# Optimization experiments

Hardware: AMD Instinct MI355X
Metric: run time of the kernel (lower is better)

Reference implementation:

```python
import jax, jax.numpy as jnp
import numpy as np

B, T, P, N, U, L, K = 32, 12, 12, 512, 64, 2, 2
C = 2 * U  # combined_dim = input_dim(rnn_units) + rnn_units = 128


def setup_inputs():
    ks = jax.random.split(jax.random.key(0), 24)
    inp = {
        'x': jax.random.normal(ks[0], (B, T, N, 1), jnp.float32),
        'adj': jax.random.uniform(ks[1], (N, N), jnp.float32),
        'spatial_mask_1': 0.1 * jax.random.normal(ks[2], (N, N), jnp.float32),
        'spatial_mask_2': 0.1 * jax.random.normal(ks[3], (N, N), jnp.float32),
        'temporal_mask': 0.1 * jax.random.normal(ks[4], (T, N), jnp.float32),
        'fc_in_w': 0.1 * jax.random.normal(ks[5], (1, U), jnp.float32),
        'fc_in_b': jnp.zeros((U,), jnp.float32),
        'fc_out_w': 0.1 * jax.random.normal(ks[6], (U, 1), jnp.float32),
        'fc_out_b': jnp.zeros((1,), jnp.float32),
    }
    i = 7
    for pre in ('enc', 'dec'):
        for name, od in (('w_ru', 2 * U), ('w_c', U), ('w_ru2', 2 * U), ('w_c2', U)):
            inp[pre + '_' + name] = 0.08 * jax.random.normal(ks[i], (L, 2 * K, C, od), jnp.float32)
            i += 1
            inp[pre + '_' + name.replace('w', 'b')] = jnp.zeros((L, od), jnp.float32)
    return inp


def _supports(adj):
    # adj_hat = A + I; fwd = D_out^-1 A_hat ; bwd = D_in^-1 A_hat^T (inf -> 0)
    ah = adj + jnp.eye(adj.shape[0], dtype=adj.dtype)
    d_out = ah.sum(1)
    d_in = ah.sum(0)
    inv_out = jnp.where(d_out > 0, 1.0 / d_out, 0.0)
    inv_in = jnp.where(d_in > 0, 1.0 / d_in, 0.0)
    return inv_out[:, None] * ah, inv_in[:, None] * ah.T


def _dgc(x, sup, w, b):
    # x: [B,N,C]; sup: (fwd,bwd) each [N,N]; w: [2K,C,O]; b: [O]
    # The torch code expands x K times per support, so each k-slice of x_out is
    # identical: sum_k P_s @ w[k] == P_s @ w[sK:(s+1)K].sum(0). Same math, fused.
    pf = jnp.einsum('nm,bni->bmi', sup[0], x)
    pb = jnp.einsum('nm,bni->bmi', sup[1], x)
    return (jnp.einsum('bni,io->bno', pf, w[:K].sum(0))
            + jnp.einsum('bni,io->bno', pb, w[K:].sum(0)) + b)


def _cell(x, h, s1, s2, w_ru, b_ru, w_c, b_c, w_ru2, b_ru2, w_c2, b_c2):
    xh = jnp.concatenate([x, h], axis=-1)
    r1, u1 = jnp.split(jax.nn.sigmoid(_dgc(xh, s1, w_ru, b_ru)), 2, axis=-1)
    c1 = jnp.tanh(_dgc(jnp.concatenate([x, r1 * h], axis=-1), s1, w_c, b_c))
    r2, u2 = jnp.split(jax.nn.sigmoid(_dgc(xh, s2, w_ru2, b_ru2)), 2, axis=-1)
    c2 = jnp.tanh(_dgc(jnp.concatenate([x, r2 * h], axis=-1), s2, w_c2, b_c2))
    u = 0.5 * (u1 + u2)
    c = 0.5 * (c1 + c2)
    return (1.0 - u) * h + u * c


def _forward(x, adj, sm1, sm2, tm, fc_in_w, fc_in_b, fc_out_w, fc_out_b, enc, dec):
    x = x * (jnp.tanh(tm) + 1.0)[None, :, :, None]
    adj1 = adj * (jnp.tanh(0.5 * (sm1 + sm1.T)) + 1.0)
    adj2 = adj * (jnp.tanh(0.5 * (sm2 + sm2.T)) + 1.0)
    s1 = _supports(adj1)
    s2 = _supports(adj2)

    def run_layers(cells, inp, h):
        hs = []
        for i in range(L):
            hi = _cell(inp, h[i], s1, s2, *[p[i] for p in cells])
            hs.append(hi)
            inp = hi
        return jnp.stack(hs)

    def enc_step(h, xt):
        inp = xt @ fc_in_w + fc_in_b  # [B,N,U]
        return run_layers(enc, inp, h), None

    h0 = jnp.zeros((L, B, N, U), x.dtype)
    h, _ = jax.lax.scan(enc_step, h0, jnp.swapaxes(x, 0, 1))

    def dec_step(carry, _):
        h, go = carry
        inp = go @ fc_in_w + fc_in_b
        h = run_layers(dec, inp, h)
        out_t = h[-1] @ fc_out_w + fc_out_b  # [B,N,1]
        return (h, out_t), out_t

    _, outs = jax.lax.scan(dec_step, (h, jnp.zeros((B, N, 1), x.dtype)), None, length=P)
    return jnp.swapaxes(outs, 0, 1)[..., 0]  # [B,P,N]


def reference(x, adj, spatial_mask_1, spatial_mask_2, temporal_mask,
              fc_in_w, fc_in_b, fc_out_w, fc_out_b,
              enc_w_ru, enc_b_ru, enc_w_c, enc_b_c, enc_w_ru2, enc_b_ru2, enc_w_c2, enc_b_c2,
              dec_w_ru, dec_b_ru, dec_w_c, dec_b_c, dec_w_ru2, dec_b_ru2, dec_w_c2, dec_b_c2):
    enc = (enc_w_ru, enc_b_ru, enc_w_c, enc_b_c, enc_w_ru2, enc_b_ru2, enc_w_c2, enc_b_c2)
    dec = (dec_w_ru, dec_b_ru, dec_w_c, dec_b_c, dec_w_ru2, dec_b_ru2, dec_w_c2, dec_b_c2)
    return _forward(x, adj, spatial_mask_1, spatial_mask_2, temporal_mask,
                    fc_in_w, fc_in_b, fc_out_w, fc_out_b, enc, dec)
```

## Files before the change

kernel.cpp:

```cpp
#include <hip/hip_runtime.h>
#include <math.h>

#define NN 512
#define BB 32
#define UU 64
#define CC 128
#define TT 12
#define NP 12
#define RRR (NN*BB)

typedef _Float16 f16;
typedef f16 f16x8 __attribute__((ext_vector_type(8)));
typedef f16 f16x4 __attribute__((ext_vector_type(4)));
typedef float f32x4 __attribute__((ext_vector_type(4)));

__device__ __forceinline__ void gload16(const f16* g, f16* l) {
  __builtin_amdgcn_global_load_lds((const __attribute__((address_space(1))) void*)g,
                                   (__attribute__((address_space(3))) void*)l, 16, 0, 0);
}

static const size_t OFF_ST    = 0;
static const size_t OFF_AH    = OFF_ST   + (size_t)4*512*512;
static const size_t OFF_INVD  = OFF_AH   + (size_t)2*512*512;
static const size_t OFF_XH    = OFF_INVD + 2048;
static const size_t OFF_H     = OFF_XH   + (size_t)2*RRR*CC;
static const size_t OFF_RH    = OFF_H    + (size_t)2*RRR*UU;
static const size_t OFF_U     = OFF_RH   + (size_t)2*RRR*UU;
static const size_t OFF_CB    = OFF_U    + (size_t)2*RRR*UU;
static const size_t OFF_F16   = OFF_CB   + (size_t)2*RRR*UU;
static const size_t OFF_ST16A = OFF_F16;
static const size_t OFF_ST16B = OFF_ST16A + 524288;
static const size_t OFF_XHT1  = OFF_ST16B + 524288;
static const size_t OFF_XHT2  = OFF_XHT1  + 1048576;
static const size_t OFF_RHT1  = OFF_XHT2  + 1048576;
static const size_t OFF_RHT2  = OFF_RHT1  + 1048576;
static const size_t OFF_P1    = OFF_RHT2  + 1048576;
static const size_t OFF_P2    = OFF_P1    + 4194304;
static const size_t OFF_Q1    = OFF_P2    + 4194304;
static const size_t OFF_Q2    = OFF_Q1    + 2097152;
static const size_t OFF_WT1   = OFF_Q2    + 2097152;
static const size_t OFF_WT2   = OFF_WT1   + 196608;

__global__ void k_build_ah(const float* __restrict__ adj, const float* __restrict__ sm1,
                           const float* __restrict__ sm2, float* __restrict__ ah) {
  int a = blockIdx.y, i = blockIdx.x;
  const float* sm = a ? sm2 : sm1;
  for (int j = threadIdx.x; j < NN; j += blockDim.x) {
    float m = tanhf(0.5f * (sm[i*NN + j] + sm[j*NN + i])) + 1.0f;
    ah[((size_t)a*NN + i)*NN + j] = adj[i*NN + j] * m + ((i == j) ? 1.0f : 0.0f);
  }
}

__global__ void k_deg(const float* __restrict__ ah, float* __restrict__ invd) {
  int a = blockIdx.y, n = blockIdx.x;
  const float* A = ah + (size_t)a*NN*NN;
  __shared__ float sr[256], sc[256];
  int t = threadIdx.x;
  sr[t] = A[(size_t)n*NN + t] + A[(size_t)n*NN + t + 256];
  sc[t] = A[(size_t)t*NN + n] + A[(size_t)(t+256)*NN + n];
  __syncthreads();
  for (int s = 128; s > 0; s >>= 1) {
    if (t < s) { sr[t] += sr[t+s]; sc[t] += sc[t+s]; }
    __syncthreads();
  }
  if (t == 0) {
    float dr = sr[0], dc = sc[0];
    invd[(a*2 + 0)*NN + n] = dr > 0.f ? 1.f/dr : 0.f;
    invd[(a*2 + 1)*NN + n] = dc > 0.f ? 1.f/dc : 0.f;
  }
}

__global__ void k_st(const float* __restrict__ ah, const float* __restrict__ invd,
                     float* __restrict__ ST) {
  int s = blockIdx.y, m = blockIdx.x;
  int a = s >> 1, dir = s & 1;
  const float* A = ah + (size_t)a*NN*NN;
  const float* inv = invd + (a*2 + dir)*NN;
  float* out = ST + ((size_t)s*NN + m)*NN;
  for (int n = threadIdx.x; n < NN; n += blockDim.x) {
    float v = dir ? A[(size_t)m*NN + n] : A[(size_t)n*NN + m];
    out[n] = inv[n] * v;
  }
}

__global__ void k_splitA(const float* __restrict__ s, f16* __restrict__ a1,
                         f16* __restrict__ a2, int total) {
  int i = blockIdx.x*blockDim.x + threadIdx.x;
  if (i >= total) return;
  float v = s[i] * 256.0f;
  f16 hi = (f16)v;
  a1[i] = hi;
  a2[i] = (f16)(v - (float)hi);
}

__global__ void k_wsumt(const float* __restrict__ w, f16* __restrict__ wt1,
                        f16* __restrict__ wt2, int O) {
  int idx = blockIdx.x*blockDim.x + threadIdx.x;
  int total = 2*2*O*128;
  if (idx >= total) return;
  int i  = idx & 127;
  int o  = (idx >> 7) % O;
  int fb = (idx / (128*O)) & 1;
  int l  = idx / (128*O*2);
  const float* wl = w + (((size_t)(l*4 + fb*2)*128 + i)*O + o);
  float v = (wl[0] + wl[(size_t)128*O]) * 256.0f;
  f16 hi = (f16)v;
  size_t dst = ((size_t)(l*2 + fb)*O + o)*128 + i;
  wt1[dst] = hi;
  wt2[dst] = (f16)(v - (float)hi);
}

__launch_bounds__(256)
__global__ void k_tsplit(const float* __restrict__ src, int lds_, long long srcZ,
                         f16* __restrict__ d1, f16* __restrict__ d2, long long dstZ) {
  __shared__ float tile[64][65];
  const float* S = src + (size_t)blockIdx.z*srcZ;
  f16* D1 = d1 + (size_t)blockIdx.z*dstZ;
  f16* D2 = d2 + (size_t)blockIdx.z*dstZ;
  int t = threadIdx.x;
  int c0 = blockIdx.x*64, k0 = blockIdx.y*64;
#pragma unroll
  for (int it = 0; it < 4; ++it) {
    int r = (t >> 4) + it*16;
    int c = (t & 15)*4;
    float4 v = *(const float4*)(S + (size_t)(k0 + r)*lds_ + c0 + c);
    tile[r][c] = v.x; tile[r][c+1] = v.y; tile[r][c+2] = v.z; tile[r][c+3] = v.w;
  }
  __syncthreads();
#pragma unroll
  for (int it = 0; it < 4; ++it) {
    int c = (t >> 4) + it*16;
    int ks = (t & 15)*4;
    f16x4 h1, h2;
#pragma unroll
    for (int j = 0; j < 4; ++j) {
      float v = tile[ks + j][c];
      f16 hi = (f16)v;
      h1[j] = hi;
      h2[j] = (f16)(v - (float)hi);
    }
    *(f16x4*)(D1 + (size_t)(c0 + c)*512 + k0 + ks) = h1;
    *(f16x4*)(D2 + (size_t)(c0 + c)*512 + k0 + ks) = h2;
  }
}

template<int MODE>
__launch_bounds__(256)
__global__ void k_mm16f(const f16* __restrict__ A1g, const f16* __restrict__ A2g, long long aZ,
                        const f16* __restrict__ B1g, const f16* __restrict__ B2g, long long bZ,
                        f16* __restrict__ C1g, f16* __restrict__ C2g, int ldc, long long cZ,
                        float scale) {
  const int bid = blockIdx.x;
  const int c = bid & 7, i = bid >> 3;
  int x, y; long long z;
  if (MODE == 0) { x = 2*c + (i & 1); y = i >> 1; z = 0; }
  else           { z = c >> 2; x = 2*(c & 3) + (i & 1); y = i >> 1; }
  const f16* A1 = A1g + z*aZ; const f16* A2 = A2g + z*aZ;
  const f16* B1 = B1g + z*bZ; const f16* B2 = B2g + z*bZ;
  f16* C1 = C1g + z*cZ; f16* C2 = C2g + z*cZ;
  const int row0 = x*128, col0 = y*128;

  __shared__ __align__(16) f16 As1[128*64], As2[128*64], Bs1[128*64], Bs2[128*64];
  const int tid = threadIdx.x;
  const int lane = tid & 63, w = tid >> 6;
  const int wr = w >> 1, wc = w & 1;
  const int rq = lane >> 3;
  const int gq = ((lane & 7) ^ rq) * 8;

  f32x4 acc[4][4];
#pragma unroll
  for (int m = 0; m < 4; ++m)
#pragma unroll
    for (int n = 0; n < 4; ++n) acc[m][n] = (f32x4){0.f,0.f,0.f,0.f};

  for (int k0 = 0; k0 < 512; k0 += 64) {
    __syncthreads();
#pragma unroll
    for (int q = 0; q < 4; ++q) {
      const int rloc = w*32 + q*8;
      gload16(A1 + (size_t)(row0 + rloc + rq)*512 + k0 + gq, As1 + rloc*64);
      gload16(A2 + (size_t)(row0 + rloc + rq)*512 + k0 + gq, As2 + rloc*64);
      gload16(B1 + (size_t)(col0 + rloc + rq)*512 + k0 + gq, Bs1 + rloc*64);
      gload16(B2 + (size_t)(col0 + rloc + rq)*512 + k0 + gq, Bs2 + rloc*64);
    }
    __syncthreads();
#pragma unroll
    for (int ks = 0; ks < 2; ++ks) {
      const int gk = ks*4 + (lane >> 4);
      f16x8 a1f[4], a2f[4], b1f[4], b2f[4];
#pragma unroll
      for (int m = 0; m < 4; ++m) {
        const int ra = wr*64 + m*16 + (lane & 15);
        const int sa = ra*64 + ((gk ^ (ra & 7))*8);
        a1f[m] = *(const f16x8*)(As1 + sa);
        a2f[m] = *(const f16x8*)(As2 + sa);
        const int rb = wc*64 + m*16 + (lane & 15);
        const int sb = rb*64 + ((gk ^ (rb & 7))*8);
        b1f[m] = *(const f16x8*)(Bs1 + sb);
        b2f[m] = *(const f16x8*)(Bs2 + sb);
      }
#pragma unroll
      for (int m = 0; m < 4; ++m)
#pragma unroll
        for (int n = 0; n < 4; ++n) {
          acc[m][n] = __builtin_amdgcn_mfma_f32_16x16x32_f16(a1f[m], b1f[n], acc[m][n], 0, 0, 0);
          acc[m][n] = __builtin_amdgcn_mfma_f32_16x16x32_f16(a1f[m], b2f[n], acc[m][n], 0, 0, 0);
          acc[m][n] = __builtin_amdgcn_mfma_f32_16x16x32_f16(a2f[m], b1f[n], acc[m][n], 0, 0, 0);
        }
    }
  }
#pragma unroll
  for (int m = 0; m < 4; ++m) {
    const int row = row0 + wr*64 + m*16 + (lane >> 4)*4;
#pragma unroll
    for (int n = 0; n < 4; ++n) {
      const int col = col0 + wc*64 + n*16 + (lane & 15);
#pragma unroll
      for (int r = 0; r < 4; ++r) {
        float v = acc[m][n][r] * scale;
        f16 hi = (f16)v;
        C1[(size_t)(row + r)*ldc + col] = hi;
        C2[(size_t)(row + r)*ldc + col] = (f16)(v - (float)hi);
      }
    }
  }
}

__launch_bounds__(256)
__global__ void k_gatesmf(const f16* __restrict__ P1, const f16* __restrict__ P2,
                          const f16* __restrict__ W1g0, const f16* __restrict__ W2g0,
                          const f16* __restrict__ W1g1, const f16* __restrict__ W2g1,
                          const float* __restrict__ b0, const float* __restrict__ b1,
                          const float* __restrict__ h,
                          float* __restrict__ rh, float* __restrict__ ubuf) {
  const int g = blockIdx.z;
  const f16* W1 = g ? W1g1 : W1g0;
  const f16* W2 = g ? W2g1 : W2g0;
  const float* bias = g ? b1 : b0;
  float* rh_g = rh   + (size_t)g * RRR * UU;
  float* u_g  = ubuf + (size_t)g * RRR * UU;
  __shared__ __align__(16) f16 As1[128*64], As2[128*64], Bs1[128*64], Bs2[128*64];
  const int tid = threadIdx.x;
  const int lane = tid & 63, w = tid >> 6;
  const int wr = w >> 1, wc = w & 1;
  const int R0 = blockIdx.x * 128;
  const int rq = lane >> 3;
  const int gq = ((lane & 7) ^ rq) * 8;

  f32x4 acc[4][4];
#pragma unroll
  for (int m = 0; m < 4; ++m)
#pragma unroll
    for (int n = 0; n < 4; ++n) acc[m][n] = (f32x4){0.f,0.f,0.f,0.f};

  for (int sup = 0; sup < 2; ++sup) {
    const f16* A1 = P1 + (size_t)(2*g + sup)*RRR*CC;
    const f16* A2 = P2 + (size_t)(2*g + sup)*RRR*CC;
    const f16* B1 = W1 + (size_t)sup*16384;
    const f16* B2 = W2 + (size_t)sup*16384;
    for (int k0 = 0; k0 < 128; k0 += 64) {
      __syncthreads();
#pragma unroll
      for (int q = 0; q < 4; ++q) {
        const int rloc = w*32 + q*8;
        gload16(A1 + (size_t)(R0 + rloc + rq)*128 + k0 + gq, As1 + rloc*64);
        gload16(A2 + (size_t)(R0 + rloc + rq)*128 + k0 + gq, As2 + rloc*64);
        gload16(B1 + (size_t)(rloc + rq)*128 + k0 + gq, Bs1 + rloc*64);
        gload16(B2 + (size_t)(rloc + rq)*128 + k0 + gq, Bs2 + rloc*64);
      }
      __syncthreads();
#pragma unroll
      for (int ks = 0; ks < 2; ++ks) {
        const int gk = ks*4 + (lane >> 4);
        f16x8 a1f[4], a2f[4], b1f[4], b2f[4];
#pragma unroll
        for (int m = 0; m < 4; ++m) {
          const int ra = wr*64 + m*16 + (lane & 15);
          const int sa = ra*64 + ((gk ^ (ra & 7))*8);
          a1f[m] = *(const f16x8*)(As1 + sa);
          a2f[m] = *(const f16x8*)(As2 + sa);
          const int rb = wc*64 + m*16 + (lane & 15);
          const int sb = rb*64 + ((gk ^ (rb & 7))*8);
          b1f[m] = *(const f16x8*)(Bs1 + sb);
          b2f[m] = *(const f16x8*)(Bs2 + sb);
        }
#pragma unroll
        for (int m = 0; m < 4; ++m)
#pragma unroll
          for (int n = 0; n < 4; ++n) {
            acc[m][n] = __builtin_amdgcn_mfma_f32_16x16x32_f16(a1f[m], b1f[n], acc[m][n], 0, 0, 0);
            acc[m][n] = __builtin_amdgcn_mfma_f32_16x16x32_f16(a1f[m], b2f[n], acc[m][n], 0, 0, 0);
            acc[m][n] = __builtin_amdgcn_mfma_f32_16x16x32_f16(a2f[m], b1f[n], acc[m][n], 0, 0, 0);
          }
      }
    }
  }
#pragma unroll
  for (int m = 0; m < 4; ++m) {
    const int row = R0 + wr*64 + m*16 + (lane >> 4)*4;
#pragma unroll
    for (int n = 0; n < 4; ++n) {
      const int o = wc*64 + n*16 + (lane & 15);
#pragma unroll
      for (int r = 0; r < 4; ++r) {
        const int R = row + r;
        float v = acc[m][n][r] * 0.00390625f + bias[o];
        float sg = 1.f / (1.f + expf(-v));
        if (o < 64) rh_g[(size_t)R*UU + o] = sg * h[(size_t)R*UU + o];
        else        u_g[(size_t)R*UU + o - 64] = sg;
      }
    }
  }
}

__launch_bounds__(256)
__global__ void k_candmf(const f16* __restrict__ P1, const f16* __restrict__ P2,
                         const f16* __restrict__ Q1, const f16* __restrict__ Q2,
                         const f16* __restrict__ Wc1g0, const f16* __restrict__ Wc2g0,
                         const f16* __restrict__ Wc1g1, const f16* __restrict__ Wc2g1,
                         const float* __restrict__ b0, const float* __restrict__ b1,
                         float* __restrict__ cbuf) {
  const int g = blockIdx.z;
  const f16* W1 = g ? Wc1g1 : Wc1g0;
  const f16* W2 = g ? Wc2g1 : Wc2g0;
  const float* bias = g ? b1 : b0;
  float* c_g = cbuf + (size_t)g * RRR * UU;
  __shared__ __align__(16) f16 As1[128*64], As2[128*64], Bs1[64*64], Bs2[64*64];
  const int tid = threadIdx.x;
  const int lane = tid & 63, w = tid >> 6;
  const int R0 = blockIdx.x * 128;
  const int rq = lane >> 3;
  const int gq = ((lane & 7) ^ rq) * 8;

  f32x4 acc[2][4];
#pragma unroll
  for (int m = 0; m < 2; ++m)
#pragma unroll
    for (int n = 0; n < 4; ++n) acc[m][n] = (f32x4){0.f,0.f,0.f,0.f};

  for (int seg = 0; seg < 4; ++seg) {
    const int sup = seg >> 1, isQ = seg & 1;
    const f16* A1 = isQ ? (Q1 + ((size_t)g*2 + sup)*1048576)
                        : (P1 + (size_t)(2*g + sup)*RRR*CC);
    const f16* A2 = isQ ? (Q2 + ((size_t)g*2 + sup)*1048576)
                        : (P2 + (size_t)(2*g + sup)*RRR*CC);
    const int lda = isQ ? 64 : 128;
    const f16* B1 = W1 + (size_t)sup*8192 + (isQ ? 64 : 0);
    const f16* B2 = W2 + (size_t)sup*8192 + (isQ ? 64 : 0);
    __syncthreads();
#pragma unroll
    for (int q = 0; q < 4; ++q) {
      const int rloc = w*32 + q*8;
      gload16(A1 + (size_t)(R0 + rloc + rq)*lda + gq, As1 + rloc*64);
      gload16(A2 + (size_t)(R0 + rloc + rq)*lda + gq, As2 + rloc*64);
    }
#pragma unroll
    for (int q = 0; q < 2; ++q) {
      const int rloc = w*16 + q*8;
      gload16(B1 + (size_t)(rloc + rq)*128 + gq, Bs1 + rloc*64);
      gload16(B2 + (size_t)(rloc + rq)*128 + gq, Bs2 + rloc*64);
    }
    __syncthreads();
#pragma unroll
    for (int ks = 0; ks < 2; ++ks) {
      const int gk = ks*4 + (lane >> 4);
      f16x8 a1f[2], a2f[2], b1f[4], b2f[4];
#pragma unroll
      for (int m = 0; m < 2; ++m) {
        const int ra = w*32 + m*16 + (lane & 15);
        const int sa = ra*64 + ((gk ^ (ra & 7))*8);
        a1f[m] = *(const f16x8*)(As1 + sa);
        a2f[m] = *(const f16x8*)(As2 + sa);
      }
#pragma unroll
      for (int n = 0; n < 4; ++n) {
        const int rb = n*16 + (lane & 15);
        const int sb = rb*64 + ((gk ^ (rb & 7))*8);
        b1f[n] = *(const f16x8*)(Bs1 + sb);
        b2f[n] = *(const f16x8*)(Bs2 + sb);
      }
#pragma unroll
      for (int m = 0; m < 2; ++m)
#pragma unroll
        for (int n = 0; n < 4; ++n) {
          acc[m][n] = __builtin_amdgcn_mfma_f32_16x16x32_f16(a1f[m], b1f[n], acc[m][n], 0, 0, 0);
          acc[m][n] = __builtin_amdgcn_mfma_f32_16x16x32_f16(a1f[m], b2f[n], acc[m][n], 0, 0, 0);
          acc[m][n] = __builtin_amdgcn_mfma_f32_16x16x32_f16(a2f[m], b1f[n], acc[m][n], 0, 0, 0);
        }
    }
  }
#pragma unroll
  for (int m = 0; m < 2; ++m) {
    const int row = R0 + w*32 + m*16 + (lane >> 4)*4;
#pragma unroll
    for (int n = 0; n < 4; ++n) {
      const int o = n*16 + (lane & 15);
#pragma unroll
      for (int r = 0; r < 4; ++r)
        c_g[(size_t)(row + r)*UU + o] = tanhf(acc[m][n][r] * 0.00390625f + bias[o]);
    }
  }
}

__global__ void k_xin(const float* __restrict__ x, const float* __restrict__ tm,
                      const float* __restrict__ fiw, const float* __restrict__ fib,
                      float* __restrict__ xh0, int t) {
  int idx = blockIdx.x*blockDim.x + threadIdx.x;
  int u = idx & 63, R = idx >> 6;
  int b = R & 31, n = R >> 5;
  float xs = x[((size_t)b*TT + t)*NN + n] * (tanhf(tm[t*NN + n]) + 1.0f);
  xh0[(size_t)R*CC + u] = xs * fiw[u] + fib[u];
}

__global__ void k_decin0(const float* __restrict__ fib, float* __restrict__ xh0) {
  int idx = blockIdx.x*blockDim.x + threadIdx.x;
  int u = idx & 63, R = idx >> 6;
  xh0[(size_t)R*CC + u] = fib[u];
}

__global__ void k_update(const float* __restrict__ u1, const float* __restrict__ u2,
                         const float* __restrict__ c1, const float* __restrict__ c2,
                         float* __restrict__ h, float* __restrict__ xh,
                         float* __restrict__ xh_next) {
  int idx = blockIdx.x*blockDim.x + threadIdx.x;
  int R = idx >> 6, o = idx & 63;
  float u = 0.5f*(u1[idx] + u2[idx]);
  float c = 0.5f*(c1[idx] + c2[idx]);
  float hn = (1.f - u)*h[idx] + u*c;
  h[idx] = hn;
  xh[(size_t)R*CC + 64 + o] = hn;
  if (xh_next) xh_next[(size_t)R*CC + o] = hn;
}

__global__ void k_out(const float* __restrict__ h1, const float* __restrict__ fow,
                      const float* __restrict__ fob, const float* __restrict__ fiw,
                      const float* __restrict__ fib, float* __restrict__ out,
                      float* __restrict__ xh0, int p) {
  int R = blockIdx.x*blockDim.x + threadIdx.x;
  int b = R & 31, n = R >> 5;
  const float* hr = h1 + (size_t)R*UU;
  float s = fob[0];
#pragma unroll
  for (int u = 0; u < UU; ++u) s = fmaf(hr[u], fow[u], s);
  out[(size_t)b*(NP*NN) + (size_t)p*NN + n] = s;
#pragma unroll
  for (int u = 0; u < UU; ++u) xh0[(size_t)R*CC + u] = fmaf(s, fiw[u], fib[u]);
}

extern "C" void kernel_launch(void* const* d_in, const int* in_sizes, int n_in,
                              void* d_out, int out_size, void* d_ws, size_t ws_size,
                              hipStream_t stream) {
  (void)in_sizes; (void)n_in; (void)out_size; (void)ws_size;
  const float* x   = (const float*)d_in[0];
  const float* adj = (const float*)d_in[1];
  const float* sm1 = (const float*)d_in[2];
  const float* sm2 = (const float*)d_in[3];
  const float* tm  = (const float*)d_in[4];
  const float* fiw = (const float*)d_in[5];
  const float* fib = (const float*)d_in[6];
  const float* fow = (const float*)d_in[7];
  const float* fob = (const float*)d_in[8];

  float* WS   = (float*)d_ws;
  float* ST   = WS + OFF_ST;
  float* AH   = WS + OFF_AH;
  float* INVD = WS + OFF_INVD;
  float* XH   = WS + OFF_XH;
  float* H    = WS + OFF_H;
  float* RH   = WS + OFF_RH;
  float* Ubuf = WS + OFF_U;
  float* Cbuf = WS + OFF_CB;
  f16* ST1  = (f16*)(WS + OFF_ST16A);
  f16* ST2  = (f16*)(WS + OFF_ST16B);
  f16* XHT1 = (f16*)(WS + OFF_XHT1);
  f16* XHT2 = (f16*)(WS + OFF_XHT2);
  f16* RHT1 = (f16*)(WS + OFF_RHT1);
  f16* RHT2 = (f16*)(WS + OFF_RHT2);
  f16* P1   = (f16*)(WS + OFF_P1);
  f16* P2   = (f16*)(WS + OFF_P2);
  f16* Q1   = (f16*)(WS + OFF_Q1);
  f16* Q2   = (f16*)(WS + OFF_Q2);
  f16* WT1  = (f16*)(WS + OFF_WT1);
  f16* WT2  = (f16*)(WS + OFF_WT2);

  k_build_ah<<<dim3(512,2),256,0,stream>>>(adj, sm1, sm2, AH);
  k_deg<<<dim3(512,2),256,0,stream>>>(AH, INVD);
  k_st<<<dim3(512,4),256,0,stream>>>(AH, INVD, ST);
  k_splitA<<<4096,256,0,stream>>>(ST, ST1, ST2, 2048*512);

  const int widx[8] = {9, 11, 13, 15, 17, 19, 21, 23};
  const int Osz[8]  = {128, 64, 128, 64, 128, 64, 128, 64};
  const size_t woff16[8] = {0, 65536, 98304, 163840, 196608, 262144, 294912, 360448};
  for (int tau = 0; tau < 8; ++tau) {
    int total = 2*2*Osz[tau]*128;
    k_wsumt<<<(total + 255)/256, 256, 0, stream>>>((const float*)d_in[widx[tau]],
                                                   WT1 + woff16[tau], WT2 + woff16[tau],
                                                   Osz[tau]);
  }

  hipMemsetAsync(XH, 0, (size_t)2*RRR*CC*sizeof(float), stream);
  hipMemsetAsync(H,  0, (size_t)2*RRR*UU*sizeof(float), stream);

  const float inv256 = 1.0f/256.0f;

  for (int step = 0; step < TT + NP; ++step) {
    const bool enc = step < TT;
    const int ph = enc ? 0 : 1;
    if (enc)             k_xin<<<4096,256,0,stream>>>(x, tm, fiw, fib, XH, step);
    else if (step == TT) k_decin0<<<4096,256,0,stream>>>(fib, XH);

    for (int l = 0; l < 2; ++l) {
      float* xh_l = XH + (size_t)l*RRR*CC;
      float* h_l  = H  + (size_t)l*RRR*UU;
      const size_t lru = (size_t)l*2*128*128;
      const size_t lc  = (size_t)l*2*64*128;
      const f16* Wru1a = WT1 + woff16[ph*4+0] + lru;
      const f16* Wru2a = WT2 + woff16[ph*4+0] + lru;
      const f16* Wru1b = WT1 + woff16[ph*4+2] + lru;
      const f16* Wru2b = WT2 + woff16[ph*4+2] + lru;
      const f16* Wc1a  = WT1 + woff16[ph*4+1] + lc;
      const f16* Wc2a  = WT2 + woff16[ph*4+1] + lc;
      const f16* Wc1b  = WT1 + woff16[ph*4+3] + lc;
      const f16* Wc2b  = WT2 + woff16[ph*4+3] + lc;
      const float* bru  = (const float*)d_in[enc?10:18] + (size_t)l*128;
      const float* bc   = (const float*)d_in[enc?12:20] + (size_t)l*64;
      const float* bru2 = (const float*)d_in[enc?14:22] + (size_t)l*128;
      const float* bc2  = (const float*)d_in[enc?16:24] + (size_t)l*64;

      k_tsplit<<<dim3(64,8,1),256,0,stream>>>(xh_l, 4096, 0, XHT1, XHT2, 0);
      k_mm16f<0><<<512,256,0,stream>>>(ST1, ST2, 0, XHT1, XHT2, 0,
                                       P1, P2, 4096, 0, inv256);
      k_gatesmf<<<dim3(128,1,2),256,0,stream>>>(P1, P2, Wru1a, Wru2a, Wru1b, Wru2b,
                                                bru, bru2, h_l, RH, Ubuf);
      k_tsplit<<<dim3(32,8,2),256,0,stream>>>(RH, 2048, (long long)RRR*UU,
                                              RHT1, RHT2, (long long)2048*512);
      k_mm16f<1><<<256,256,0,stream>>>(ST1, ST2, (long long)1024*512,
                                       RHT1, RHT2, (long long)2048*512,
                                       Q1, Q2, 2048, (long long)1024*2048, inv256);
      k_candmf<<<dim3(128,1,2),256,0,stream>>>(P1, P2, Q1, Q2, Wc1a, Wc2a, Wc1b, Wc2b,
                                               bc, bc2, Cbuf);
      k_update<<<4096,256,0,stream>>>(Ubuf, Ubuf + (size_t)RRR*UU,
                                      Cbuf, Cbuf + (size_t)RRR*UU,
                                      h_l, xh_l, (l == 0) ? (XH + (size_t)RRR*CC) : nullptr);
    }
    if (!enc) {
      int p = step - TT;
      k_out<<<64,256,0,stream>>>(H + (size_t)RRR*UU, fow, fob, fiw, fib,
                                 (float*)d_out, XH, p);
    }
  }
}
```

Measured before the change: 5.354 ms.

## Double-buffer LDS tiles in GEMM kernels and fuse candidate with GRU update

Converts the three MFMA GEMM kernels to double-buffered LDS staging. The next k-tile is loaded asynchronously while the current one is computed, with one vmcnt wait and barrier per step instead of two syncthreads. It also merges the candidate GEMM and the elementwise GRU update into one kernel that computes both gates per 64-row tile and writes h directly, removing the Cbuf round trip and a launch. This doubles the LDS use per block, which may lower occupancy.

```diff
diff --git a/kernel.cpp b/kernel.cpp
--- a/kernel.cpp
+++ b/kernel.cpp
@@ -17,6 +17,10 @@
 __device__ __forceinline__ void gload16(const f16* g, f16* l) {
   __builtin_amdgcn_global_load_lds((const __attribute__((address_space(1))) void*)g,
                                    (__attribute__((address_space(3))) void*)l, 16, 0, 0);
+}
+__device__ __forceinline__ void pipe_fence() {
+  asm volatile("s_waitcnt vmcnt(0)" ::: "memory");
+  __builtin_amdgcn_s_barrier();
 }
 
 static const size_t OFF_ST    = 0;
@@ -160,7 +164,7 @@
   f16* C1 = C1g + z*cZ; f16* C2 = C2g + z*cZ;
   const int row0 = x*128, col0 = y*128;
 
-  __shared__ __align__(16) f16 As1[128*64], As2[128*64], Bs1[128*64], Bs2[128*64];
+  __shared__ __align__(16) f16 As1[2][128*64], As2[2][128*64], Bs1[2][128*64], Bs2[2][128*64];
   const int tid = threadIdx.x;
   const int lane = tid & 63, w = tid >> 6;
   const int wr = w >> 1, wc = w & 1;
@@ -173,17 +177,24 @@
 #pragma unroll
     for (int n = 0; n < 4; ++n) acc[m][n] = (f32x4){0.f,0.f,0.f,0.f};
 
-  for (int k0 = 0; k0 < 512; k0 += 64) {
-    __syncthreads();
+  auto STAGE = [&](int t, int bsel) {
+    const int k0 = t*64;
 #pragma unroll
     for (int q = 0; q < 4; ++q) {
       const int rloc = w*32 + q*8;
-      gload16(A1 + (size_t)(row0 + rloc + rq)*512 + k0 + gq, As1 + rloc*64);
-      gload16(A2 + (size_t)(row0 + rloc + rq)*512 + k0 + gq, As2 + rloc*64);
-      gload16(B1 + (size_t)(col0 + rloc + rq)*512 + k0 + gq, Bs1 + rloc*64);
-      gload16(B2 + (size_t)(col0 + rloc + rq)*512 + k0 + gq, Bs2 + rloc*64);
-    }
-    __syncthreads();
+      gload16(A1 + (size_t)(row0 + rloc + rq)*512 + k0 + gq, As1[bsel] + rloc*64);
+      gload16(A2 + (size_t)(row0 + rloc + rq)*512 + k0 + gq, As2[bsel] + rloc*64);
+      gload16(B1 + (size_t)(col0 + rloc + rq)*512 + k0 + gq, Bs1[bsel] + rloc*64);
+      gload16(B2 + (size_t)(col0 + rloc + rq)*512 + k0 + gq, Bs2[bsel] + rloc*64);
+    }
+  };
+
+  STAGE(0, 0);
+  pipe_fence();
+#pragma unroll
+  for (int t = 0; t < 8; ++t) {
+    const int cur = t & 1;
+    if (t < 7) STAGE(t + 1, cur ^ 1);
 #pragma unroll
     for (int ks = 0; ks < 2; ++ks) {
       const int gk = ks*4 + (lane >> 4);
@@ -192,12 +203,12 @@
       for (int m = 0; m < 4; ++m) {
         const int ra = wr*64 + m*16 + (lane & 15);
         const int sa = ra*64 + ((gk ^ (ra & 7))*8);
-        a1f[m] = *(const f16x8*)(As1 + sa);
-        a2f[m] = *(const f16x8*)(As2 + sa);
+        a1f[m] = *(const f16x8*)(As1[cur] + sa);
+        a2f[m] = *(const f16x8*)(As2[cur] + sa);
         const int rb = wc*64 + m*16 + (lane & 15);
         const int sb = rb*64 + ((gk ^ (rb & 7))*8);
-        b1f[m] = *(const f16x8*)(Bs1 + sb);
-        b2f[m] = *(const f16x8*)(Bs2 + sb);
+        b1f[m] = *(const f16x8*)(Bs1[cur] + sb);
+        b2f[m] = *(const f16x8*)(Bs2[cur] + sb);
       }
 #pragma unroll
       for (int m = 0; m < 4; ++m)
@@ -208,6 +219,7 @@
           acc[m][n] = __builtin_amdgcn_mfma_f32_16x16x32_f16(a2f[m], b1f[n], acc[m][n], 0, 0, 0);
         }
     }
+    pipe_fence();
   }
 #pragma unroll
   for (int m = 0; m < 4; ++m) {
@@ -239,7 +251,7 @@
   const float* bias = g ? b1 : b0;
   float* rh_g = rh   + (size_t)g * RRR * UU;
   float* u_g  = ubuf + (size_t)g * RRR * UU;
-  __shared__ __align__(16) f16 As1[128*64], As2[128*64], Bs1[128*64], Bs2[128*64];
+  __shared__ __align__(16) f16 As1[2][128*64], As2[2][128*64], Bs1[2][128*64], Bs2[2][128*64];
   const int tid = threadIdx.x;
   const int lane = tid & 63, w = tid >> 6;
   const int wr = w >> 1, wc = w & 1;
@@ -253,47 +265,53 @@
 #pragma unroll
     for (int n = 0; n < 4; ++n) acc[m][n] = (f32x4){0.f,0.f,0.f,0.f};
 
-  for (int sup = 0; sup < 2; ++sup) {
+  auto STAGE = [&](int s, int bsel) {
+    const int sup = s >> 1, k0 = (s & 1)*64;
     const f16* A1 = P1 + (size_t)(2*g + sup)*RRR*CC;
     const f16* A2 = P2 + (size_t)(2*g + sup)*RRR*CC;
     const f16* B1 = W1 + (size_t)sup*16384;
     const f16* B2 = W2 + (size_t)sup*16384;
-    for (int k0 = 0; k0 < 128; k0 += 64) {
-      __syncthreads();
-#pragma unroll
-      for (int q = 0; q < 4; ++q) {
-        const int rloc = w*32 + q*8;
-        gload16(A1 + (size_t)(R0 + rloc + rq)*128 + k0 + gq, As1 + rloc*64);
-        gload16(A2 + (size_t)(R0 + rloc + rq)*128 + k0 + gq, As2 + rloc*64);
-        gload16(B1 + (size_t)(rloc + rq)*128 + k0 + gq, Bs1 + rloc*64);
-        gload16(B2 + (size_t)(rloc + rq)*128 + k0 + gq, Bs2 + rloc*64);
+#pragma unroll
+    for (int q = 0; q < 4; ++q) {
+      const int rloc = w*32 + q*8;
+      gload16(A1 + (size_t)(R0 + rloc + rq)*128 + k0 + gq, As1[bsel] + rloc*64);
+      gload16(A2 + (size_t)(R0 + rloc + rq)*128 + k0 + gq, As2[bsel] + rloc*64);
+      gload16(B1 + (size_t)(rloc + rq)*128 + k0 + gq, Bs1[bsel] + rloc*64);
+      gload16(B2 + (size_t)(rloc + rq)*128 + k0 + gq, Bs2[bsel] + rloc*64);
+    }
+  };
+
+  STAGE(0, 0);
+  pipe_fence();
+#pragma unroll
+  for (int s = 0; s < 4; ++s) {
+    const int cur = s & 1;
+    if (s < 3) STAGE(s + 1, cur ^ 1);
+#pragma unroll
+    for (int ks = 0; ks < 2; ++ks) {
+      const int gk = ks*4 + (lane >> 4);
+      f16x8 a1f[4], a2f[4], b1f[4], b2f[4];
+#pragma unroll
+      for (int m = 0; m < 4; ++m) {
+        const int ra = wr*64 + m*16 + (lane & 15);
+        const int sa = ra*64 + ((gk ^ (ra & 7))*8);
+        a1f[m] = *(const f16x8*)(As1[cur] + sa);
+        a2f[m] = *(const f16x8*)(As2[cur] + sa);
+        const int rb = wc*64 + m*16 + (lane & 15);
+        const int sb = rb*64 + ((gk ^ (rb & 7))*8);
+        b1f[m] = *(const f16x8*)(Bs1[cur] + sb);
+        b2f[m] = *(const f16x8*)(Bs2[cur] + sb);
       }
-      __syncthreads();
-#pragma unroll
-      for (int ks = 0; ks < 2; ++ks) {
-        const int gk = ks*4 + (lane >> 4);
-        f16x8 a1f[4], a2f[4], b1f[4], b2f[4];
-#pragma unroll
-        for (int m = 0; m < 4; ++m) {
-          const int ra = wr*64 + m*16 + (lane & 15);
-          const int sa = ra*64 + ((gk ^ (ra & 7))*8);
-          a1f[m] = *(const f16x8*)(As1 + sa);
-          a2f[m] = *(const f16x8*)(As2 + sa);
-          const int rb = wc*64 + m*16 + (lane & 15);
-          const int sb = rb*64 + ((gk ^ (rb & 7))*8);
-          b1f[m] = *(const f16x8*)(Bs1 + sb);
-          b2f[m] = *(const f16x8*)(Bs2 + sb);
+#pragma unroll
+      for (int m = 0; m < 4; ++m)
+#pragma unroll
+        for (int n = 0; n < 4; ++n) {
+          acc[m][n] = __builtin_amdgcn_mfma_f32_16x16x32_f16(a1f[m], b1f[n], acc[m][n], 0, 0, 0);
+          acc[m][n] = __builtin_amdgcn_mfma_f32_16x16x32_f16(a1f[m], b2f[n], acc[m][n], 0, 0, 0);
+          acc[m][n] = __builtin_amdgcn_mfma_f32_16x16x32_f16(a2f[m], b1f[n], acc[m][n], 0, 0, 0);
         }
-#pragma unroll
-        for (int m = 0; m < 4; ++m)
-#pragma unroll
-          for (int n = 0; n < 4; ++n) {
-            acc[m][n] = __builtin_amdgcn_mfma_f32_16x16x32_f16(a1f[m], b1f[n], acc[m][n], 0, 0, 0);
-            acc[m][n] = __builtin_amdgcn_mfma_f32_16x16x32_f16(a1f[m], b2f[n], acc[m][n], 0, 0, 0);
-            acc[m][n] = __builtin_amdgcn_mfma_f32_16x16x32_f16(a2f[m], b1f[n], acc[m][n], 0, 0, 0);
-          }
-      }
-    }
+    }
+    pipe_fence();
   }
 #pragma unroll
   for (int m = 0; m < 4; ++m) {
@@ -314,90 +332,95 @@
 }
 
 __launch_bounds__(256)
-__global__ void k_candmf(const f16* __restrict__ P1, const f16* __restrict__ P2,
-                         const f16* __restrict__ Q1, const f16* __restrict__ Q2,
-                         const f16* __restrict__ Wc1g0, const f16* __restrict__ Wc2g0,
-                         const f16* __restrict__ Wc1g1, const f16* __restrict__ Wc2g1,
-                         const float* __restrict__ b0, const float* __restrict__ b1,
-                         float* __restrict__ cbuf) {
-  const int g = blockIdx.z;
-  const f16* W1 = g ? Wc1g1 : Wc1g0;
-  const f16* W2 = g ? Wc2g1 : Wc2g0;
-  const float* bias = g ? b1 : b0;
-  float* c_g = cbuf + (size_t)g * RRR * UU;
-  __shared__ __align__(16) f16 As1[128*64], As2[128*64], Bs1[64*64], Bs2[64*64];
+__global__ void k_candupd(const f16* __restrict__ P1, const f16* __restrict__ P2,
+                          const f16* __restrict__ Q1, const f16* __restrict__ Q2,
+                          const f16* __restrict__ Wc1g0, const f16* __restrict__ Wc2g0,
+                          const f16* __restrict__ Wc1g1, const f16* __restrict__ Wc2g1,
+                          const float* __restrict__ b0, const float* __restrict__ b1,
+                          const float* __restrict__ ubuf,
+                          float* __restrict__ h, float* __restrict__ xh,
+                          float* __restrict__ xh_next) {
+  __shared__ __align__(16) f16 As1[2][64*64], As2[2][64*64], Bs1[2][64*64], Bs2[2][64*64];
   const int tid = threadIdx.x;
   const int lane = tid & 63, w = tid >> 6;
-  const int R0 = blockIdx.x * 128;
+  const int R0 = blockIdx.x * 64;
   const int rq = lane >> 3;
   const int gq = ((lane & 7) ^ rq) * 8;
 
   f32x4 acc[2][4];
 #pragma unroll
-  for (int m = 0; m < 2; ++m)
-#pragma unroll
-    for (int n = 0; n < 4; ++n) acc[m][n] = (f32x4){0.f,0.f,0.f,0.f};
-
-  for (int seg = 0; seg < 4; ++seg) {
+  for (int g = 0; g < 2; ++g)
+#pragma unroll
+    for (int n = 0; n < 4; ++n) acc[g][n] = (f32x4){0.f,0.f,0.f,0.f};
+
+  auto STAGE = [&](int s, int bsel) {
+    const int g = s >> 2, seg = s & 3;
     const int sup = seg >> 1, isQ = seg & 1;
     const f16* A1 = isQ ? (Q1 + ((size_t)g*2 + sup)*1048576)
                         : (P1 + (size_t)(2*g + sup)*RRR*CC);
     const f16* A2 = isQ ? (Q2 + ((size_t)g*2 + sup)*1048576)
                         : (P2 + (size_t)(2*g + sup)*RRR*CC);
     const int lda = isQ ? 64 : 128;
+    const f16* W1 = g ? Wc1g1 : Wc1g0;
+    const f16* W2 = g ? Wc2g1 : Wc2g0;
     const f16* B1 = W1 + (size_t)sup*8192 + (isQ ? 64 : 0);
     const f16* B2 = W2 + (size_t)sup*8192 + (isQ ? 64 : 0);
-    __syncthreads();
-#pragma unroll
-    for (int q = 0; q < 4; ++q) {
-      const int rloc = w*32 + q*8;
-      gload16(A1 + (size_t)(R0 + rloc + rq)*lda + gq, As1 + rloc*64);
-      gload16(A2 + (size_t)(R0 + rloc + rq)*lda + gq, As2 + rloc*64);
-    }
 #pragma unroll
     for (int q = 0; q < 2; ++q) {
       const int rloc = w*16 + q*8;
-      gload16(B1 + (size_t)(rloc + rq)*128 + gq, Bs1 + rloc*64);
-      gload16(B2 + (size_t)(rloc + rq)*128 + gq, Bs2 + rloc*64);
-    }
-    __syncthreads();
+      gload16(A1 + (size_t)(R0 + rloc + rq)*lda + gq, As1[bsel] + rloc*64);
+      gload16(A2 + (size_t)(R0 + rloc + rq)*lda + gq, As2[bsel] + rloc*64);
+      gload16(B1 + (size_t)(rloc + rq)*128 + gq, Bs1[bsel] + rloc*64);
+      gload16(B2 + (size_t)(rloc + rq)*128 + gq, Bs2[bsel] + rloc*64);
+    }
+  };
+
+  STAGE(0, 0);
+  pipe_fence();
+#pragma unroll
+  for (int s = 0; s < 8; ++s) {
+    const int cur = s & 1;
+    const int g = s >> 2;
+    if (s < 7) STAGE(s + 1, cur ^ 1);
 #pragma unroll
     for (int ks = 0; ks < 2; ++ks) {
       const int gk = ks*4 + (lane >> 4);
-      f16x8 a1f[2], a2f[2], b1f[4], b2f[4];
-#pragma unroll
-      for (int m = 0; m < 2; ++m) {
-        const int ra = w*32 + m*16 + (lane & 15);
-        const int sa = ra*64 + ((gk ^ (ra & 7))*8);
-        a1f[m] = *(const f16x8*)(As1 + sa);
-        a2f[m] = *(const f16x8*)(As2 + sa);
-      }
+      const int ra = w*16 + (lane & 15);
+      const int sa = ra*64 + ((gk ^ (ra & 7))*8);
+      f16x8 a1f = *(const f16x8*)(As1[cur] + sa);
+      f16x8 a2f = *(const f16x8*)(As2[cur] + sa);
+      f16x8 b1f[4], b2f[4];
 #pragma unroll
       for (int n = 0; n < 4; ++n) {
         const int rb = n*16 + (lane & 15);
         const int sb = rb*64 + ((gk ^ (rb & 7))*8);
-        b1f[n] = *(const f16x8*)(Bs1 + sb);
-        b2f[n] = *(const f16x8*)(Bs2 + sb);
+        b1f[n] = *(const f16x8*)(Bs1[cur] + sb);
+        b2f[n] = *(const f16x8*)(Bs2[cur] + sb);
       }
 #pragma unroll
-      for (int m = 0; m < 2; ++m)
-#pragma unroll
-        for (int n = 0; n < 4; ++n) {
-          acc[m][n] = __builtin_amdgcn_mfma_f32_16x16x32_f16(a1f[m], b1f[n], acc[m][n], 0, 0, 0);
-          acc[m][n] = __builtin_amdgcn_mfma_f32_16x16x32_f16(a1f[m], b2f[n], acc[m][n], 0, 0, 0);
-          acc[m][n] = __builtin_amdgcn_mfma_f32_16x16x32_f16(a2f[m], b1f[n], acc[m][n], 0, 0, 0);
-        }
-    }
-  }
-#pragma unroll
-  for (int m = 0; m < 2; ++m) {
-    const int row = R0 + w*32 + m*16 + (lane >> 4)*4;
-#pragma unroll
-    for (int n = 0; n < 4; ++n) {
-      const int o = n*16 + (lane & 15);
-#pragma unroll
-      for (int r = 0; r < 4; ++r)
-        c_g[(size_t)(row + r)*UU + o] = tanhf(acc[m][n][r] * 0.00390625f + bias[o]);
+      for (int n = 0; n < 4; ++n) {
+        acc[g][n] = __builtin_amdgcn_mfma_f32_16x16x32_f16(a1f, b1f[n], acc[g][n], 0, 0, 0);
+        acc[g][n] = __builtin_amdgcn_mfma_f32_16x16x32_f16(a1f, b2f[n], acc[g][n], 0, 0, 0);
+        acc[g][n] = __builtin_amdgcn_mfma_f32_16x16x32_f16(a2f, b1f[n], acc[g][n], 0, 0, 0);
+      }
+    }
+    pipe_fence();
+  }
+#pragma unroll
+  for (int n = 0; n < 4; ++n) {
+    const int o = n*16 + (lane & 15);
+#pragma unroll
+    for (int r = 0; r < 4; ++r) {
+      const int R = R0 + w*16 + (lane >> 4)*4 + r;
+      const size_t idx = (size_t)R*UU + o;
+      float c1 = tanhf(acc[0][n][r] * 0.00390625f + b0[o]);
+      float c2 = tanhf(acc[1][n][r] * 0.00390625f + b1[o]);
+      float u = 0.5f*(ubuf[idx] + ubuf[(size_t)RRR*UU + idx]);
+      float cc = 0.5f*(c1 + c2);
+      float hn = (1.f - u)*h[idx] + u*cc;
+      h[idx] = hn;
+      xh[(size_t)R*CC + 64 + o] = hn;
+      if (xh_next) xh_next[(size_t)R*CC + o] = hn;
     }
   }
 }
@@ -416,20 +439,6 @@
   int idx = blockIdx.x*blockDim.x + threadIdx.x;
   int u = idx & 63, R = idx >> 6;
   xh0[(size_t)R*CC + u] = fib[u];
-}
-
-__global__ void k_update(const float* __restrict__ u1, const float* __restrict__ u2,
-                         const float* __restrict__ c1, const float* __restrict__ c2,
-                         float* __restrict__ h, float* __restrict__ xh,
-                         float* __restrict__ xh_next) {
-  int idx = blockIdx.x*blockDim.x + threadIdx.x;
-  int R = idx >> 6, o = idx & 63;
-  float u = 0.5f*(u1[idx] + u2[idx]);
-  float c = 0.5f*(c1[idx] + c2[idx]);
-  float hn = (1.f - u)*h[idx] + u*c;
-  h[idx] = hn;
-  xh[(size_t)R*CC + 64 + o] = hn;
-  if (xh_next) xh_next[(size_t)R*CC + o] = hn;
 }
 
 __global__ void k_out(const float* __restrict__ h1, const float* __restrict__ fow,
@@ -469,7 +478,6 @@
   float* H    = WS + OFF_H;
   float* RH   = WS + OFF_RH;
   float* Ubuf = WS + OFF_U;
-  float* Cbuf = WS + OFF_CB;
   f16* ST1  = (f16*)(WS + OFF_ST16A);
   f16* ST2  = (f16*)(WS + OFF_ST16B);
   f16* XHT1 = (f16*)(WS + OFF_XHT1);
@@ -537,11 +545,9 @@
       k_mm16f<1><<<256,256,0,stream>>>(ST1, ST2, (long long)1024*512,
                                        RHT1, RHT2, (long long)2048*512,
                                        Q1, Q2, 2048, (long long)1024*2048, inv256);
-      k_candmf<<<dim3(128,1,2),256,0,stream>>>(P1, P2, Q1, Q2, Wc1a, Wc2a, Wc1b, Wc2b,
-                                               bc, bc2, Cbuf);
-      k_update<<<4096,256,0,stream>>>(Ubuf, Ubuf + (size_t)RRR*UU,
-                                      Cbuf, Cbuf + (size_t)RRR*UU,
-                                      h_l, xh_l, (l == 0) ? (XH + (size_t)RRR*CC) : nullptr);
+      k_candupd<<<256,256,0,stream>>>(P1, P2, Q1, Q2, Wc1a, Wc2a, Wc1b, Wc2b,
+                                      bc, bc2, Ubuf, h_l, xh_l,
+                                      (l == 0) ? (XH + (size_t)RRR*CC) : nullptr);
     }
     if (!enc) {
       int p = step - TT;
```

Measured after the change: 5.988 ms. 1.12x slower.
